# Kernel optimization log

Hardware: AMD Instinct MI355X
Metric: run time of the kernel (lower is better)

The kernel has to match this reference:

```python
import jax, jax.numpy as jnp
import numpy as np

NEG_INF = -1e30  # stands in for -math.inf in masked_fill; -inf itself also works in fp32


def setup_inputs() -> dict:
    key = jax.random.key(0)
    k1, k2, k3, k4, k5 = jax.random.split(key, 5)
    B, T, S, H = 32, 512, 1024, 1024
    query = jax.random.normal(k1, (B, T, H), dtype=jnp.float32)
    encoder_outputs = jax.random.normal(k2, (S, B, H), dtype=jnp.float32)  # seq-first, as in torch RNN outputs
    src_lengths = jax.random.randint(k3, (B,), 1, S + 1, dtype=jnp.int32)
    W_in = jax.random.normal(k4, (H, H), dtype=jnp.float32) / np.sqrt(H)
    W_out = jax.random.normal(k5, (H, 2 * H), dtype=jnp.float32) / np.sqrt(2 * H)
    b_out = jnp.zeros((H,), dtype=jnp.float32)
    return {"query": query, "encoder_outputs": encoder_outputs, "src_lengths": src_lengths,
            "W_in": W_in, "W_out": W_out, "b_out": b_out}


def reference(query, encoder_outputs, src_lengths, W_in, W_out, b_out):
    # query: [B,T,H]; encoder_outputs: [S,B,H] (seq-first)
    # NOTE: the original module computes a length mask but never applies it;
    # instead it fills positions where the raw score is exactly 0 with -inf.
    z = jnp.einsum('bth,ih->bti', query, W_in)                 # linear_in (no bias)
    scores = jnp.einsum('bti,sbi->bts', z, encoder_outputs)    # bmm -> [B,T,S]
    scores = jnp.where(scores == 0, jnp.float32(-jnp.inf), scores)
    p = jax.nn.softmax(scores, axis=2)                         # [B,T,S]
    c = jnp.einsum('bts,sbh->bth', p, encoder_outputs)         # context [B,T,H]
    cat = jnp.concatenate([c, query], axis=2)                  # [B,T,2H]
    attn_h_t = jnp.tanh(jnp.einsum('btk,hk->bth', cat, W_out) + b_out)
    return attn_h_t
```

## Files before the change

kernel.cpp:

```cpp
#include <hip/hip_runtime.h>
#include <math.h>


__device__ inline unsigned short f2bf(float x) {
    unsigned int u = __float_as_uint(x);
    u += 0x7fffu + ((u >> 16) & 1u);
    return (unsigned short)(u >> 16);
}
__device__ inline float bf2f(unsigned short h) {
    return __uint_as_float(((unsigned int)h) << 16);
}

typedef __attribute__((ext_vector_type(8))) short short8;
typedef __attribute__((ext_vector_type(4))) float f32x4;

__device__ inline void gld_lds16(const void* g, void* l) {
    __builtin_amdgcn_global_load_lds(
        (const __attribute__((address_space(1))) unsigned int*)g,
        (__attribute__((address_space(3))) unsigned int*)l, 16, 0, 0);
}

__device__ inline short8 frag_ld(const short* Ls, int rowbase, int ks8, int lane) {
    const int r = lane & 15;
    const int q = lane >> 4;
    return *(const short8*)&Ls[(rowbase + r) * 64 + (((ks8 + q) ^ (r & 7)) << 3)];
}

template<int NCHUNK, int OUT_MODE>
__global__ __launch_bounds__(256, 2)
void gemm_mfma(const unsigned short* __restrict__ A0, const unsigned short* __restrict__ A1,
               const unsigned short* __restrict__ A2,
               const unsigned short* __restrict__ B0, const unsigned short* __restrict__ B1,
               const unsigned short* __restrict__ B2,
               float* __restrict__ Of, unsigned short* __restrict__ Oh,
               unsigned short* __restrict__ Ol, const float* __restrict__ bias,
               int chunkK, long lda, long ldb, long ldc, long sA, long sB, long sC)
{
    __shared__ short As[128 * 64];
    __shared__ short Bs[128 * 64];

    const int tid  = threadIdx.x;
    const int wave = tid >> 6, lane = tid & 63;
    const int wm = (wave & 1) << 6, wn = (wave >> 1) << 6;
    const long m0 = (long)blockIdx.y * 128, n0 = (long)blockIdx.x * 128;
    const int bz = blockIdx.z;

    const unsigned short* Ap[3] = {A0, A1, A2};
    const unsigned short* Bp[3] = {B0, B1, B2};

    f32x4 acc[4][4];
#pragma unroll
    for (int i = 0; i < 4; ++i)
#pragma unroll
        for (int j = 0; j < 4; ++j) acc[i][j] = (f32x4){0.f, 0.f, 0.f, 0.f};

    const int lr   = lane >> 3;
    const int gran = (lane & 7) ^ lr;
    const int rw   = wave * 32;

#pragma unroll
    for (int c = 0; c < NCHUNK; ++c) {
        const unsigned short* Ac = Ap[c] + (long)bz * sA + m0 * lda;
        const unsigned short* Bc = Bp[c] + (long)bz * sB + n0 * ldb;
        for (int k0 = 0; k0 < chunkK; k0 += 64) {
            __syncthreads();
#pragma unroll
            for (int seg = 0; seg < 4; ++seg) {
                const int row = rw + seg * 8 + lr;
                gld_lds16(Ac + (long)row * lda + k0 + (gran << 3),
                          As + (rw + seg * 8) * 64);
            }
#pragma unroll
            for (int seg = 0; seg < 4; ++seg) {
                const int row = rw + seg * 8 + lr;
                gld_lds16(Bc + (long)row * ldb + k0 + (gran << 3),
                          Bs + (rw + seg * 8) * 64);
            }
            __syncthreads();
#pragma unroll
            for (int ks = 0; ks < 2; ++ks) {
                short8 af[4], bfv[4];
#pragma unroll
                for (int i = 0; i < 4; ++i) af[i]  = frag_ld(As, wm + i * 16, ks * 4, lane);
#pragma unroll
                for (int j = 0; j < 4; ++j) bfv[j] = frag_ld(Bs, wn + j * 16, ks * 4, lane);
#pragma unroll
                for (int i = 0; i < 4; ++i)
#pragma unroll
                    for (int j = 0; j < 4; ++j)
                        acc[i][j] = __builtin_amdgcn_mfma_f32_16x16x32_bf16(
                            af[i], bfv[j], acc[i][j], 0, 0, 0);
            }
        }
    }

    const int q = lane >> 4, r = lane & 15;
#pragma unroll
    for (int i = 0; i < 4; ++i) {
#pragma unroll
        for (int rr = 0; rr < 4; ++rr) {
            const long grow = m0 + wm + i * 16 + q * 4 + rr;
#pragma unroll
            for (int j = 0; j < 4; ++j) {
                const long gcol = n0 + wn + j * 16 + r;
                const float v = acc[i][j][rr];
                const long off = (long)bz * sC + grow * ldc + gcol;
                if constexpr (OUT_MODE == 0) {
                    Oh[off] = f2bf(v);
                } else if constexpr (OUT_MODE == 1) {
                    unsigned short h = f2bf(v);
                    Oh[off] = h;
                    Ol[off] = f2bf(v - bf2f(h));
                } else if constexpr (OUT_MODE == 2) {
                    Of[off] = v;
                } else {
                    Of[off] = tanhf(v + bias[gcol]);
                }
            }
        }
    }
}

template<bool HAS_LO>
__global__ __launch_bounds__(256)
void split_f32_bf16(const float* __restrict__ x, unsigned short* __restrict__ hi,
                    unsigned short* __restrict__ lo, int n4)
{
    const int i = blockIdx.x * 256 + threadIdx.x;
    if (i >= n4) return;
    const float4 v = ((const float4*)x)[i];
    ushort4 h;
    h.x = f2bf(v.x); h.y = f2bf(v.y); h.z = f2bf(v.z); h.w = f2bf(v.w);
    ((ushort4*)hi)[i] = h;
    if constexpr (HAS_LO) {
        ushort4 l;
        l.x = f2bf(v.x - bf2f(h.x)); l.y = f2bf(v.y - bf2f(h.y));
        l.z = f2bf(v.z - bf2f(h.z)); l.w = f2bf(v.w - bf2f(h.w));
        ((ushort4*)lo)[i] = l;
    }
}

__global__ __launch_bounds__(256)
void transpose_enc(const unsigned short* __restrict__ E, unsigned short* __restrict__ ET)
{
    __shared__ unsigned short L[64][72];
    const int s0 = blockIdx.x * 64, h0 = blockIdx.y * 64, b = blockIdx.z;
    const int tid = threadIdx.x;
#pragma unroll
    for (int io = 0; io < 2; ++io) {
        const int g = io * 256 + tid;
        const int rs = g >> 3, c8 = (g & 7) * 8;
        const unsigned short* src = E + ((long)(s0 + rs) * 32 + b) * 1024 + h0 + c8;
        *(ushort4*)&L[rs][c8]     = *(const ushort4*)(src);
        *(ushort4*)&L[rs][c8 + 4] = *(const ushort4*)(src + 4);
    }
    __syncthreads();
#pragma unroll
    for (int io = 0; io < 2; ++io) {
        const int g = io * 256 + tid;
        const int rh = g >> 3, c8 = (g & 7) * 8;
        unsigned short t[8];
#pragma unroll
        for (int j = 0; j < 8; ++j) t[j] = L[c8 + j][rh];
        unsigned short* dst = ET + ((long)b * 1024 + h0 + rh) * 1024 + s0 + c8;
        *(ushort4*)(dst)     = *(const ushort4*)&t[0];
        *(ushort4*)(dst + 4) = *(const ushort4*)&t[4];
    }
}

__global__ __launch_bounds__(256)
void softmax_p_bf16(const float* __restrict__ P, unsigned short* __restrict__ Pb)
{
    const int row  = blockIdx.x * 4 + (threadIdx.x >> 6);
    const int lane = threadIdx.x & 63;
    const float* p = P + (long)row * 1024 + lane * 4;
    unsigned short* pb = Pb + (long)row * 1024 + lane * 4;

    float4 v[4];
    float mx = -INFINITY;
#pragma unroll
    for (int i = 0; i < 4; ++i) {
        v[i] = *(const float4*)(p + i * 256);
        v[i].x = (v[i].x == 0.f) ? -INFINITY : v[i].x;
        v[i].y = (v[i].y == 0.f) ? -INFINITY : v[i].y;
        v[i].z = (v[i].z == 0.f) ? -INFINITY : v[i].z;
        v[i].w = (v[i].w == 0.f) ? -INFINITY : v[i].w;
        mx = fmaxf(mx, fmaxf(fmaxf(v[i].x, v[i].y), fmaxf(v[i].z, v[i].w)));
    }
#pragma unroll
    for (int o = 32; o > 0; o >>= 1) mx = fmaxf(mx, __shfl_xor(mx, o, 64));

    float sum = 0.f;
#pragma unroll
    for (int i = 0; i < 4; ++i) {
        v[i].x = __expf(v[i].x - mx);
        v[i].y = __expf(v[i].y - mx);
        v[i].z = __expf(v[i].z - mx);
        v[i].w = __expf(v[i].w - mx);
        sum += v[i].x + v[i].y + v[i].z + v[i].w;
    }
#pragma unroll
    for (int o = 32; o > 0; o >>= 1) sum += __shfl_xor(sum, o, 64);

    const float inv = 1.f / sum;
#pragma unroll
    for (int i = 0; i < 4; ++i) {
        ushort4 u;
        u.x = f2bf(v[i].x * inv); u.y = f2bf(v[i].y * inv);
        u.z = f2bf(v[i].z * inv); u.w = f2bf(v[i].w * inv);
        *(ushort4*)(pb + i * 256) = u;
    }
}

#define BM 128
#define BN 128
#define BKT 16

template<bool BT, bool DO_TANH, bool CAT_A>
__global__ __launch_bounds__(256)
void sgemm(const float* __restrict__ A, const float* __restrict__ A2,
           const float* __restrict__ Bmat, const float* __restrict__ bias,
           float* __restrict__ C,
           int M, int N, int K, int Ksplit,
           int lda, int ldb, int ldc,
           long sA, long sB, long sC)
{
    __shared__ float Asb[BKT][BM];
    __shared__ float Bsb[BKT][BN];

    const int bz = blockIdx.z;
    const float* Ab = A + (long)bz * sA;
    const float* Bb = Bmat + (long)bz * sB;
    float* Cb = C + (long)bz * sC;

    const int tid = threadIdx.x;
    const int m0 = blockIdx.y * BM;
    const int n0 = blockIdx.x * BN;
    const int tx = tid & 15;
    const int ty = tid >> 4;

    float acc[8][8];
#pragma unroll
    for (int i = 0; i < 8; ++i)
#pragma unroll
        for (int j = 0; j < 8; ++j) acc[i][j] = 0.f;

    for (int kk = 0; kk < K; kk += BKT) {
        const float* Asrc = Ab;
        int acol = kk;
        if constexpr (CAT_A) {
            if (kk >= Ksplit) { Asrc = A2; acol = kk - Ksplit; }
        }
#pragma unroll
        for (int i = 0; i < 2; ++i) {
            int f = i * 256 + tid;
            int row = f >> 2;
            int k4 = (f & 3) << 2;
            float4 v = *(const float4*)(Asrc + (long)(m0 + row) * lda + acol + k4);
            Asb[k4 + 0][row] = v.x; Asb[k4 + 1][row] = v.y;
            Asb[k4 + 2][row] = v.z; Asb[k4 + 3][row] = v.w;
        }
        if constexpr (BT) {
#pragma unroll
            for (int i = 0; i < 2; ++i) {
                int f = i * 256 + tid;
                int row = f >> 2;
                int k4 = (f & 3) << 2;
                float4 v = *(const float4*)(Bb + (long)(n0 + row) * ldb + kk + k4);
                Bsb[k4 + 0][row] = v.x; Bsb[k4 + 1][row] = v.y;
                Bsb[k4 + 2][row] = v.z; Bsb[k4 + 3][row] = v.w;
            }
        } else {
#pragma unroll
            for (int i = 0; i < 2; ++i) {
                int f = i * 256 + tid;
                int kr = f >> 5;
                int n4 = (f & 31) << 2;
                float4 v = *(const float4*)(Bb + (long)(kk + kr) * ldb + n0 + n4);
                *(float4*)&Bsb[kr][n4] = v;
            }
        }
        __syncthreads();
#pragma unroll
        for (int k = 0; k < BKT; ++k) {
            float a[8], bv[8];
            *(float4*)&a[0]  = *(const float4*)&Asb[k][ty * 4];
            *(float4*)&a[4]  = *(const float4*)&Asb[k][ty * 4 + 64];
            *(float4*)&bv[0] = *(const float4*)&Bsb[k][tx * 4];
            *(float4*)&bv[4] = *(const float4*)&Bsb[k][tx * 4 + 64];
#pragma unroll
            for (int i = 0; i < 8; ++i)
#pragma unroll
                for (int j = 0; j < 8; ++j)
                    acc[i][j] = fmaf(a[i], bv[j], acc[i][j]);
        }
        __syncthreads();
    }
#pragma unroll
    for (int i = 0; i < 8; ++i) {
        int rrow = m0 + ty * 4 + (i & 3) + ((i >> 2) << 6);
        float* crow = Cb + (long)rrow * ldc;
#pragma unroll
        for (int jj = 0; jj < 2; ++jj) {
            int c0 = n0 + tx * 4 + jj * 64;
            float4 v;
            v.x = acc[i][jj * 4 + 0]; v.y = acc[i][jj * 4 + 1];
            v.z = acc[i][jj * 4 + 2]; v.w = acc[i][jj * 4 + 3];
            if constexpr (DO_TANH) {
                v.x = tanhf(v.x + bias[c0 + 0]); v.y = tanhf(v.y + bias[c0 + 1]);
                v.z = tanhf(v.z + bias[c0 + 2]); v.w = tanhf(v.w + bias[c0 + 3]);
            }
            *(float4*)(crow + c0) = v;
        }
    }
}

__global__ __launch_bounds__(256)
void softmax_rows(float* __restrict__ P)
{
    const int row = blockIdx.x * 4 + (threadIdx.x >> 6);
    const int lane = threadIdx.x & 63;
    float* p = P + (long)row * 1024 + lane * 4;
    float4 v[4];
    float mx = -INFINITY;
#pragma unroll
    for (int i = 0; i < 4; ++i) {
        v[i] = *(const float4*)(p + i * 256);
        v[i].x = (v[i].x == 0.f) ? -INFINITY : v[i].x;
        v[i].y = (v[i].y == 0.f) ? -INFINITY : v[i].y;
        v[i].z = (v[i].z == 0.f) ? -INFINITY : v[i].z;
        v[i].w = (v[i].w == 0.f) ? -INFINITY : v[i].w;
        mx = fmaxf(mx, fmaxf(fmaxf(v[i].x, v[i].y), fmaxf(v[i].z, v[i].w)));
    }
#pragma unroll
    for (int o = 32; o > 0; o >>= 1) mx = fmaxf(mx, __shfl_xor(mx, o, 64));
    float sum = 0.f;
#pragma unroll
    for (int i = 0; i < 4; ++i) {
        v[i].x = __expf(v[i].x - mx); v[i].y = __expf(v[i].y - mx);
        v[i].z = __expf(v[i].z - mx); v[i].w = __expf(v[i].w - mx);
        sum += v[i].x + v[i].y + v[i].z + v[i].w;
    }
#pragma unroll
    for (int o = 32; o > 0; o >>= 1) sum += __shfl_xor(sum, o, 64);
    const float inv = 1.f / sum;
#pragma unroll
    for (int i = 0; i < 4; ++i) {
        v[i].x *= inv; v[i].y *= inv; v[i].z *= inv; v[i].w *= inv;
        *(float4*)(p + i * 256) = v[i];
    }
}

extern "C" void kernel_launch(void* const* d_in, const int* in_sizes, int n_in,
                              void* d_out, int out_size, void* d_ws, size_t ws_size,
                              hipStream_t stream)
{
    (void)in_sizes; (void)n_in; (void)out_size;
    const int Bv = 32, T = 512, S = 1024, H = 1024;

    const float* q     = (const float*)d_in[0];
    const float* enc   = (const float*)d_in[1];
    const float* W_in  = (const float*)d_in[3];
    const float* W_out = (const float*)d_in[4];
    const float* b_out = (const float*)d_in[5];
    float* out = (float*)d_out;

    const size_t need = 264ull << 20;
    if (ws_size >= need) {
        char* w = (char*)d_ws;
        unsigned short* q_hi  = (unsigned short*)(w);
        unsigned short* q_lo  = (unsigned short*)(w + (32ull << 20));
        unsigned short* z_hi  = (unsigned short*)(w + (64ull << 20));
        unsigned short* z_lo  = (unsigned short*)(w + (96ull << 20));
        unsigned short* e_hi  = (unsigned short*)(w + (128ull << 20));
        unsigned short* e_lo  = (unsigned short*)(w + (192ull << 20));
        unsigned short* Wi_hi = (unsigned short*)(w + (256ull << 20));
        unsigned short* Wi_lo = (unsigned short*)(w + (258ull << 20));
        unsigned short* Wo_hi = (unsigned short*)(w + (260ull << 20));

        split_f32_bf16<true ><<<16384, 256, 0, stream>>>(q, q_hi, q_lo, 4194304);
        split_f32_bf16<true ><<<1024,  256, 0, stream>>>(W_in, Wi_hi, Wi_lo, 262144);
        split_f32_bf16<false><<<2048,  256, 0, stream>>>(W_out, Wo_hi, nullptr, 524288);
        split_f32_bf16<true ><<<32768, 256, 0, stream>>>(enc, e_hi, e_lo, 8388608);

        gemm_mfma<3, 1><<<dim3(8, 128, 1), 256, 0, stream>>>(
            q_hi, q_hi, q_lo, Wi_hi, Wi_lo, Wi_hi,
            nullptr, z_hi, z_lo, nullptr,
            1024, 1024, 1024, 1024, 0, 0, 0);

        gemm_mfma<3, 2><<<dim3(8, 4, 32), 256, 0, stream>>>(
            z_hi, z_hi, z_lo, e_hi, e_lo, e_hi,
            (float*)d_out, nullptr, nullptr, nullptr,
            1024, 1024, (long)Bv * H, 1024,
            (long)T * H, (long)H, (long)T * S);

        softmax_p_bf16<<<(Bv * T) / 4, 256, 0, stream>>>((const float*)d_out, q_lo);

        transpose_enc<<<dim3(16, 16, 32), 256, 0, stream>>>(e_hi, e_lo);

        gemm_mfma<1, 0><<<dim3(8, 4, 32), 256, 0, stream>>>(
            q_lo, nullptr, nullptr, e_lo, nullptr, nullptr,
            nullptr, z_hi, nullptr, nullptr,
            1024, 1024, 1024, 1024,
            (long)T * S, (long)H * S, (long)T * H);

        gemm_mfma<2, 3><<<dim3(8, 128, 1), 256, 0, stream>>>(
            z_hi, q_hi, nullptr, Wo_hi, Wo_hi + 1024, nullptr,
            (float*)d_out, nullptr, nullptr, b_out,
            1024, 1024, 2048, 1024, 0, 0, 0);
    } else {
        float* Z = (float*)d_ws;
        float* P = Z + (size_t)Bv * T * H;
        dim3 blk(256);
        sgemm<true, false, false><<<dim3(H / BN, (Bv * T) / BM, 1), blk, 0, stream>>>(
            q, nullptr, W_in, nullptr, Z,
            Bv * T, H, H, 0, H, H, H, 0, 0, 0);
        sgemm<true, false, false><<<dim3(S / BN, T / BM, Bv), blk, 0, stream>>>(
            Z, nullptr, enc, nullptr, P,
            T, S, H, 0, H, Bv * H, S, (long)T * H, H, (long)T * S);
        softmax_rows<<<(Bv * T) / 4, blk, 0, stream>>>(P);
        sgemm<false, false, false><<<dim3(H / BN, T / BM, Bv), blk, 0, stream>>>(
            P, nullptr, enc, nullptr, Z,
            T, H, S, 0, S, Bv * H, H, (long)T * S, H, (long)T * H);
        sgemm<true, true, true><<<dim3(H / BN, (Bv * T) / BM, 1), blk, 0, stream>>>(
            Z, q, W_out, b_out, out,
            Bv * T, H, 2 * H, H, H, 2 * H, H, 0, 0, 0);
    }
}
```

Measured before the change: 758.3 us.

## Fuse bf16x3 split chunks into one pass and switch later GEMMs to fp16

The three-term bf16 split GEMMs now stage hi and lo tiles of A and B together in one K loop, reusing the hi fragments across the three MFMA products. Before, each product was a separate pass that reloaded its own tiles. The context and output GEMMs now use fp16 MFMA instead of bf16, with P, encoder, query and W_out converted to fp16 for better mantissa precision. This adds an extra conversion pass over the query and converts the encoder transpose directly from fp32. It also doubles LDS use per block in the split GEMM, which may lower occupancy.

```diff
diff --git a/kernel.cpp b/kernel.cpp
--- a/kernel.cpp
+++ b/kernel.cpp
@@ -10,9 +10,14 @@
 __device__ inline float bf2f(unsigned short h) {
     return __uint_as_float(((unsigned int)h) << 16);
 }
-
-typedef __attribute__((ext_vector_type(8))) short short8;
-typedef __attribute__((ext_vector_type(4))) float f32x4;
+__device__ inline unsigned short f2h(float x) {
+    _Float16 h = (_Float16)x;
+    return *(unsigned short*)&h;
+}
+
+typedef __attribute__((ext_vector_type(8))) short    short8;
+typedef __attribute__((ext_vector_type(8))) _Float16 half8;
+typedef __attribute__((ext_vector_type(4))) float    f32x4;
 
 __device__ inline void gld_lds16(const void* g, void* l) {
     __builtin_amdgcn_global_load_lds(
@@ -21,23 +26,32 @@
 }
 
 __device__ inline short8 frag_ld(const short* Ls, int rowbase, int ks8, int lane) {
-    const int r = lane & 15;
-    const int q = lane >> 4;
+    const int r = lane & 15, q = lane >> 4;
     return *(const short8*)&Ls[(rowbase + r) * 64 + (((ks8 + q) ^ (r & 7)) << 3)];
 }
-
-template<int NCHUNK, int OUT_MODE>
+__device__ inline half8 frag_ld_h(const short* Ls, int rowbase, int ks8, int lane) {
+    const int r = lane & 15, q = lane >> 4;
+    return *(const half8*)&Ls[(rowbase + r) * 64 + (((ks8 + q) ^ (r & 7)) << 3)];
+}
+
+__device__ inline void stage_tile(const unsigned short* g, long ld, short* lds,
+                                  int rw, int lr, int gran) {
+#pragma unroll
+    for (int seg = 0; seg < 4; ++seg) {
+        const int row = rw + seg * 8 + lr;
+        gld_lds16(g + (long)row * ld + (gran << 3), lds + (rw + seg * 8) * 64);
+    }
+}
+
+template<int OUT_MODE>
 __global__ __launch_bounds__(256, 2)
-void gemm_mfma(const unsigned short* __restrict__ A0, const unsigned short* __restrict__ A1,
-               const unsigned short* __restrict__ A2,
-               const unsigned short* __restrict__ B0, const unsigned short* __restrict__ B1,
-               const unsigned short* __restrict__ B2,
-               float* __restrict__ Of, unsigned short* __restrict__ Oh,
-               unsigned short* __restrict__ Ol, const float* __restrict__ bias,
-               int chunkK, long lda, long ldb, long ldc, long sA, long sB, long sC)
-{
-    __shared__ short As[128 * 64];
-    __shared__ short Bs[128 * 64];
+void gemm_x3(const unsigned short* __restrict__ Ahg, const unsigned short* __restrict__ Alg,
+             const unsigned short* __restrict__ Bhg, const unsigned short* __restrict__ Blg,
+             float* __restrict__ Of, unsigned short* __restrict__ Oh,
+             unsigned short* __restrict__ Ol,
+             int K, long lda, long ldb, long ldc, long sA, long sB, long sC)
+{
+    __shared__ short Ah[128 * 64], Al[128 * 64], Bh[128 * 64], Bl[128 * 64];
 
     const int tid  = threadIdx.x;
     const int wave = tid >> 6, lane = tid & 63;
@@ -45,8 +59,98 @@
     const long m0 = (long)blockIdx.y * 128, n0 = (long)blockIdx.x * 128;
     const int bz = blockIdx.z;
 
-    const unsigned short* Ap[3] = {A0, A1, A2};
-    const unsigned short* Bp[3] = {B0, B1, B2};
+    const unsigned short* Ah0 = Ahg + (long)bz * sA + m0 * lda;
+    const unsigned short* Al0 = Alg + (long)bz * sA + m0 * lda;
+    const unsigned short* Bh0 = Bhg + (long)bz * sB + n0 * ldb;
+    const unsigned short* Bl0 = Blg + (long)bz * sB + n0 * ldb;
+
+    f32x4 acc[4][4];
+#pragma unroll
+    for (int i = 0; i < 4; ++i)
+#pragma unroll
+        for (int j = 0; j < 4; ++j) acc[i][j] = (f32x4){0.f, 0.f, 0.f, 0.f};
+
+    const int lr   = lane >> 3;
+    const int gran = (lane & 7) ^ lr;
+    const int rw   = wave * 32;
+
+    for (int k0 = 0; k0 < K; k0 += 64) {
+        __syncthreads();
+        stage_tile(Ah0 + k0, lda, Ah, rw, lr, gran);
+        stage_tile(Al0 + k0, lda, Al, rw, lr, gran);
+        stage_tile(Bh0 + k0, ldb, Bh, rw, lr, gran);
+        stage_tile(Bl0 + k0, ldb, Bl, rw, lr, gran);
+        __syncthreads();
+#pragma unroll
+        for (int ks = 0; ks < 2; ++ks) {
+            short8 ah[4], al[4], bh[4], bl[4];
+#pragma unroll
+            for (int i = 0; i < 4; ++i) ah[i] = frag_ld(Ah, wm + i * 16, ks * 4, lane);
+#pragma unroll
+            for (int j = 0; j < 4; ++j) bh[j] = frag_ld(Bh, wn + j * 16, ks * 4, lane);
+#pragma unroll
+            for (int i = 0; i < 4; ++i)
+#pragma unroll
+                for (int j = 0; j < 4; ++j)
+                    acc[i][j] = __builtin_amdgcn_mfma_f32_16x16x32_bf16(ah[i], bh[j], acc[i][j], 0, 0, 0);
+#pragma unroll
+            for (int j = 0; j < 4; ++j) bl[j] = frag_ld(Bl, wn + j * 16, ks * 4, lane);
+#pragma unroll
+            for (int i = 0; i < 4; ++i)
+#pragma unroll
+                for (int j = 0; j < 4; ++j)
+                    acc[i][j] = __builtin_amdgcn_mfma_f32_16x16x32_bf16(ah[i], bl[j], acc[i][j], 0, 0, 0);
+#pragma unroll
+            for (int i = 0; i < 4; ++i) al[i] = frag_ld(Al, wm + i * 16, ks * 4, lane);
+#pragma unroll
+            for (int i = 0; i < 4; ++i)
+#pragma unroll
+                for (int j = 0; j < 4; ++j)
+                    acc[i][j] = __builtin_amdgcn_mfma_f32_16x16x32_bf16(al[i], bh[j], acc[i][j], 0, 0, 0);
+        }
+    }
+
+    const int q = lane >> 4, r = lane & 15;
+#pragma unroll
+    for (int i = 0; i < 4; ++i)
+#pragma unroll
+        for (int rr = 0; rr < 4; ++rr) {
+            const long grow = m0 + wm + i * 16 + q * 4 + rr;
+#pragma unroll
+            for (int j = 0; j < 4; ++j) {
+                const long gcol = n0 + wn + j * 16 + r;
+                const float v = acc[i][j][rr];
+                const long off = (long)bz * sC + grow * ldc + gcol;
+                if constexpr (OUT_MODE == 1) {
+                    unsigned short h = f2bf(v);
+                    Oh[off] = h;
+                    Ol[off] = f2bf(v - bf2f(h));
+                } else {
+                    Of[off] = v;
+                }
+            }
+        }
+}
+
+template<int NCHUNK, int OUT_MODE>
+__global__ __launch_bounds__(256, 2)
+void gemm_f16(const unsigned short* __restrict__ A0, const unsigned short* __restrict__ A1,
+              const unsigned short* __restrict__ B0, const unsigned short* __restrict__ B1,
+              float* __restrict__ Of, unsigned short* __restrict__ Oh,
+              const float* __restrict__ bias,
+              int chunkK, long lda, long ldb, long ldc, long sA, long sB, long sC)
+{
+    __shared__ short As[128 * 64];
+    __shared__ short Bs[128 * 64];
+
+    const int tid  = threadIdx.x;
+    const int wave = tid >> 6, lane = tid & 63;
+    const int wm = (wave & 1) << 6, wn = (wave >> 1) << 6;
+    const long m0 = (long)blockIdx.y * 128, n0 = (long)blockIdx.x * 128;
+    const int bz = blockIdx.z;
+
+    const unsigned short* Ap[2] = {A0, A1};
+    const unsigned short* Bp[2] = {B0, B1};
 
     f32x4 acc[4][4];
 #pragma unroll
@@ -64,39 +168,28 @@
         const unsigned short* Bc = Bp[c] + (long)bz * sB + n0 * ldb;
         for (int k0 = 0; k0 < chunkK; k0 += 64) {
             __syncthreads();
-#pragma unroll
-            for (int seg = 0; seg < 4; ++seg) {
-                const int row = rw + seg * 8 + lr;
-                gld_lds16(Ac + (long)row * lda + k0 + (gran << 3),
-                          As + (rw + seg * 8) * 64);
+            stage_tile(Ac + k0, lda, As, rw, lr, gran);
+            stage_tile(Bc + k0, ldb, Bs, rw, lr, gran);
+            __syncthreads();
+#pragma unroll
+            for (int ks = 0; ks < 2; ++ks) {
+                half8 af[4], bfv[4];
+#pragma unroll
+                for (int i = 0; i < 4; ++i) af[i]  = frag_ld_h(As, wm + i * 16, ks * 4, lane);
+#pragma unroll
+                for (int j = 0; j < 4; ++j) bfv[j] = frag_ld_h(Bs, wn + j * 16, ks * 4, lane);
+#pragma unroll
+                for (int i = 0; i < 4; ++i)
+#pragma unroll
+                    for (int j = 0; j < 4; ++j)
+                        acc[i][j] = __builtin_amdgcn_mfma_f32_16x16x32_f16(af[i], bfv[j], acc[i][j], 0, 0, 0);
             }
-#pragma unroll
-            for (int seg = 0; seg < 4; ++seg) {
-                const int row = rw + seg * 8 + lr;
-                gld_lds16(Bc + (long)row * ldb + k0 + (gran << 3),
-                          Bs + (rw + seg * 8) * 64);
-            }
-            __syncthreads();
-#pragma unroll
-            for (int ks = 0; ks < 2; ++ks) {
-                short8 af[4], bfv[4];
-#pragma unroll
-                for (int i = 0; i < 4; ++i) af[i]  = frag_ld(As, wm + i * 16, ks * 4, lane);
-#pragma unroll
-                for (int j = 0; j < 4; ++j) bfv[j] = frag_ld(Bs, wn + j * 16, ks * 4, lane);
-#pragma unroll
-                for (int i = 0; i < 4; ++i)
-#pragma unroll
-                    for (int j = 0; j < 4; ++j)
-                        acc[i][j] = __builtin_amdgcn_mfma_f32_16x16x32_bf16(
-                            af[i], bfv[j], acc[i][j], 0, 0, 0);
-            }
         }
     }
 
     const int q = lane >> 4, r = lane & 15;
 #pragma unroll
-    for (int i = 0; i < 4; ++i) {
+    for (int i = 0; i < 4; ++i)
 #pragma unroll
         for (int rr = 0; rr < 4; ++rr) {
             const long grow = m0 + wm + i * 16 + q * 4 + rr;
@@ -106,19 +199,12 @@
                 const float v = acc[i][j][rr];
                 const long off = (long)bz * sC + grow * ldc + gcol;
                 if constexpr (OUT_MODE == 0) {
-                    Oh[off] = f2bf(v);
-                } else if constexpr (OUT_MODE == 1) {
-                    unsigned short h = f2bf(v);
-                    Oh[off] = h;
-                    Ol[off] = f2bf(v - bf2f(h));
-                } else if constexpr (OUT_MODE == 2) {
-                    Of[off] = v;
+                    Oh[off] = f2h(v);
                 } else {
                     Of[off] = tanhf(v + bias[gcol]);
                 }
             }
         }
-    }
 }
 
 template<bool HAS_LO>
@@ -141,7 +227,18 @@
 }
 
 __global__ __launch_bounds__(256)
-void transpose_enc(const unsigned short* __restrict__ E, unsigned short* __restrict__ ET)
+void conv_f32_f16(const float* __restrict__ x, unsigned short* __restrict__ o, int n4)
+{
+    const int i = blockIdx.x * 256 + threadIdx.x;
+    if (i >= n4) return;
+    const float4 v = ((const float4*)x)[i];
+    ushort4 h;
+    h.x = f2h(v.x); h.y = f2h(v.y); h.z = f2h(v.z); h.w = f2h(v.w);
+    ((ushort4*)o)[i] = h;
+}
+
+__global__ __launch_bounds__(256)
+void transpose_enc_f16(const float* __restrict__ E, unsigned short* __restrict__ ET)
 {
     __shared__ unsigned short L[64][72];
     const int s0 = blockIdx.x * 64, h0 = blockIdx.y * 64, b = blockIdx.z;
@@ -150,9 +247,13 @@
     for (int io = 0; io < 2; ++io) {
         const int g = io * 256 + tid;
         const int rs = g >> 3, c8 = (g & 7) * 8;
-        const unsigned short* src = E + ((long)(s0 + rs) * 32 + b) * 1024 + h0 + c8;
-        *(ushort4*)&L[rs][c8]     = *(const ushort4*)(src);
-        *(ushort4*)&L[rs][c8 + 4] = *(const ushort4*)(src + 4);
+        const float* src = E + ((long)(s0 + rs) * 32 + b) * 1024 + h0 + c8;
+        const float4 v0 = *(const float4*)(src);
+        const float4 v1 = *(const float4*)(src + 4);
+        L[rs][c8 + 0] = f2h(v0.x); L[rs][c8 + 1] = f2h(v0.y);
+        L[rs][c8 + 2] = f2h(v0.z); L[rs][c8 + 3] = f2h(v0.w);
+        L[rs][c8 + 4] = f2h(v1.x); L[rs][c8 + 5] = f2h(v1.y);
+        L[rs][c8 + 6] = f2h(v1.z); L[rs][c8 + 7] = f2h(v1.w);
     }
     __syncthreads();
 #pragma unroll
@@ -169,7 +270,7 @@
 }
 
 __global__ __launch_bounds__(256)
-void softmax_p_bf16(const float* __restrict__ P, unsigned short* __restrict__ Pb)
+void softmax_p_f16(const float* __restrict__ P, unsigned short* __restrict__ Pb)
 {
     const int row  = blockIdx.x * 4 + (threadIdx.x >> 6);
     const int lane = threadIdx.x & 63;
@@ -193,10 +294,8 @@
     float sum = 0.f;
 #pragma unroll
     for (int i = 0; i < 4; ++i) {
-        v[i].x = __expf(v[i].x - mx);
-        v[i].y = __expf(v[i].y - mx);
-        v[i].z = __expf(v[i].z - mx);
-        v[i].w = __expf(v[i].w - mx);
+        v[i].x = __expf(v[i].x - mx); v[i].y = __expf(v[i].y - mx);
+        v[i].z = __expf(v[i].z - mx); v[i].w = __expf(v[i].w - mx);
         sum += v[i].x + v[i].y + v[i].z + v[i].w;
     }
 #pragma unroll
@@ -206,8 +305,8 @@
 #pragma unroll
     for (int i = 0; i < 4; ++i) {
         ushort4 u;
-        u.x = f2bf(v[i].x * inv); u.y = f2bf(v[i].y * inv);
-        u.z = f2bf(v[i].z * inv); u.w = f2bf(v[i].w * inv);
+        u.x = f2h(v[i].x * inv); u.y = f2h(v[i].y * inv);
+        u.z = f2h(v[i].z * inv); u.w = f2h(v[i].w * inv);
         *(ushort4*)(pb + i * 256) = u;
     }
 }
@@ -376,37 +475,44 @@
         unsigned short* e_lo  = (unsigned short*)(w + (192ull << 20));
         unsigned short* Wi_hi = (unsigned short*)(w + (256ull << 20));
         unsigned short* Wi_lo = (unsigned short*)(w + (258ull << 20));
-        unsigned short* Wo_hi = (unsigned short*)(w + (260ull << 20));
+        unsigned short* Wo16  = (unsigned short*)(w + (260ull << 20));
+
+        unsigned short* Pb    = q_lo;
+        unsigned short* q16   = z_lo;
+        unsigned short* eT    = e_lo;
+        unsigned short* C16   = z_hi;
 
         split_f32_bf16<true ><<<16384, 256, 0, stream>>>(q, q_hi, q_lo, 4194304);
         split_f32_bf16<true ><<<1024,  256, 0, stream>>>(W_in, Wi_hi, Wi_lo, 262144);
-        split_f32_bf16<false><<<2048,  256, 0, stream>>>(W_out, Wo_hi, nullptr, 524288);
+        conv_f32_f16<<<2048, 256, 0, stream>>>(W_out, Wo16, 524288);
         split_f32_bf16<true ><<<32768, 256, 0, stream>>>(enc, e_hi, e_lo, 8388608);
 
-        gemm_mfma<3, 1><<<dim3(8, 128, 1), 256, 0, stream>>>(
-            q_hi, q_hi, q_lo, Wi_hi, Wi_lo, Wi_hi,
-            nullptr, z_hi, z_lo, nullptr,
+        gemm_x3<1><<<dim3(8, 128, 1), 256, 0, stream>>>(
+            q_hi, q_lo, Wi_hi, Wi_lo,
+            nullptr, z_hi, z_lo,
             1024, 1024, 1024, 1024, 0, 0, 0);
 
-        gemm_mfma<3, 2><<<dim3(8, 4, 32), 256, 0, stream>>>(
-            z_hi, z_hi, z_lo, e_hi, e_lo, e_hi,
-            (float*)d_out, nullptr, nullptr, nullptr,
+        gemm_x3<2><<<dim3(8, 4, 32), 256, 0, stream>>>(
+            z_hi, z_lo, e_hi, e_lo,
+            (float*)d_out, nullptr, nullptr,
             1024, 1024, (long)Bv * H, 1024,
             (long)T * H, (long)H, (long)T * S);
 
-        softmax_p_bf16<<<(Bv * T) / 4, 256, 0, stream>>>((const float*)d_out, q_lo);
-
-        transpose_enc<<<dim3(16, 16, 32), 256, 0, stream>>>(e_hi, e_lo);
-
-        gemm_mfma<1, 0><<<dim3(8, 4, 32), 256, 0, stream>>>(
-            q_lo, nullptr, nullptr, e_lo, nullptr, nullptr,
-            nullptr, z_hi, nullptr, nullptr,
+        softmax_p_f16<<<(Bv * T) / 4, 256, 0, stream>>>((const float*)d_out, Pb);
+
+        conv_f32_f16<<<16384, 256, 0, stream>>>(q, q16, 4194304);
+
+        transpose_enc_f16<<<dim3(16, 16, 32), 256, 0, stream>>>(enc, eT);
+
+        gemm_f16<1, 0><<<dim3(8, 4, 32), 256, 0, stream>>>(
+            Pb, nullptr, eT, nullptr,
+            nullptr, C16, nullptr,
             1024, 1024, 1024, 1024,
             (long)T * S, (long)H * S, (long)T * H);
 
-        gemm_mfma<2, 3><<<dim3(8, 128, 1), 256, 0, stream>>>(
-            z_hi, q_hi, nullptr, Wo_hi, Wo_hi + 1024, nullptr,
-            (float*)d_out, nullptr, nullptr, b_out,
+        gemm_f16<2, 3><<<dim3(8, 128, 1), 256, 0, stream>>>(
+            C16, q16, Wo16, Wo16 + 1024,
+            (float*)d_out, nullptr, b_out,
             1024, 1024, 2048, 1024, 0, 0, 0);
     } else {
         float* Z = (float*)d_ws;
```

Measured after the change: 725.1 us. 4.4% less time.
